# Performance work log

Measured on AMD Instinct MI355X. Metric: run time of the kernel, lower is better.

The kernel has to match this reference:

```python
import jax, jax.numpy as jnp
import numpy as np

N_NODES = 100000
N_EDGES = 3200000
IN_DIM, HID_DIM, OUT_DIM = 64, 16, 2


def setup_inputs() -> dict:
    key = jax.random.key(0)
    ks = jax.random.split(key, 6)
    x = jax.random.normal(ks[0], (N_NODES, IN_DIM), dtype=jnp.float32)
    edge_index = jax.random.randint(ks[1], (2, N_EDGES), 0, N_NODES, dtype=jnp.int64)
    W1 = jax.random.normal(ks[2], (IN_DIM, HID_DIM), dtype=jnp.float32) * (1.0 / np.sqrt(IN_DIM))
    b1 = jax.random.normal(ks[3], (HID_DIM,), dtype=jnp.float32) * 0.01
    W2 = jax.random.normal(ks[4], (HID_DIM, OUT_DIM), dtype=jnp.float32) * (1.0 / np.sqrt(HID_DIM))
    b2 = jax.random.normal(ks[5], (OUT_DIM,), dtype=jnp.float32) * 0.01
    return {"x": x, "edge_index": edge_index, "W1": W1, "b1": b1, "W2": W2, "b2": b2}


def _gcn_conv(x, src, dst, W, b, n_nodes):
    """PyG GCNConv: add self-loops, symmetric norm, linear, scatter-add, bias."""
    h = x @ W  # [N, out]
    loop = jnp.arange(n_nodes, dtype=src.dtype)
    s = jnp.concatenate([src, loop])  # [E+N]
    d = jnp.concatenate([dst, loop])
    deg = jax.ops.segment_sum(jnp.ones_like(d, dtype=h.dtype), d, num_segments=n_nodes)
    dinv = jnp.where(deg > 0, jax.lax.rsqrt(deg), 0.0)
    norm = dinv[s] * dinv[d]  # [E+N]
    msgs = h[s] * norm[:, None]  # gather + scale
    out = jax.ops.segment_sum(msgs, d, num_segments=n_nodes)
    return out + b


def reference(x, edge_index, W1, b1, W2, b2):
    src, dst = edge_index[0], edge_index[1]
    h = _gcn_conv(x, src, dst, W1, b1, N_NODES)
    h = jax.nn.relu(h)
    h = _gcn_conv(h, src, dst, W2, b2, N_NODES)
    return jax.nn.log_softmax(h, axis=1)
```

## Files before the change

### kernel.cpp

```cpp
#include <hip/hip_runtime.h>
#include <math.h>
#include <stdint.h>

#define N_NODES 100000
#define N_EDGES 3200000
#define IN_DIM  64
#define HID     16
#define OUTD    2

#define NPAD    100352
#define B_CHUNKS 128
#define CHUNK_E  (N_EDGES / B_CHUNKS)
#define NB       256
#define BK_NODES (NPAD / NB)
#define BK_CAP   14336

#define OFF_DINV  0
#define OFF_RS    (OFF_DINV + NPAD)
#define OFF_RE    (OFF_RS + NPAD)
#define OFF_H1    (OFF_RE + NPAD)
#define OFF_H2    (OFF_H1 + N_NODES * HID)
#define OFF_CSR   (OFF_H2 + N_NODES * OUTD)
#define OFF_PAIRS (OFF_CSR + N_EDGES)
#define OFF_HCNT  (OFF_PAIRS + 2 * N_EDGES)
#define OFF_BST   (OFF_HCNT + B_CHUNKS * NB)


__global__ __launch_bounds__(256) void k_bhist(const int* __restrict__ dst,
                                               unsigned* __restrict__ hcnt) {
    __shared__ unsigned h[NB];
    h[threadIdx.x] = 0u;
    __syncthreads();
    int base = blockIdx.x * CHUNK_E;
    for (int i = threadIdx.x; i < CHUNK_E; i += 256)
        atomicAdd(&h[dst[base + i] / BK_NODES], 1u);
    __syncthreads();
    hcnt[blockIdx.x * NB + threadIdx.x] = h[threadIdx.x];
}

__global__ __launch_bounds__(256) void k_bscan(unsigned* __restrict__ hcnt,
                                               int* __restrict__ bstart) {
    int bk = threadIdx.x, lane = bk & 63, wid = bk >> 6;
    int tot = 0;
    for (int b = 0; b < B_CHUNKS; b++) tot += (int)hcnt[(size_t)b * NB + bk];
    int x = tot;
#pragma unroll
    for (int off = 1; off < 64; off <<= 1) {
        int y = __shfl_up(x, off, 64);
        if (lane >= off) x += y;
    }
    __shared__ int wt[4];
    if (lane == 63) wt[wid] = x;
    __syncthreads();
    int wb = 0;
#pragma unroll
    for (int w = 0; w < 4; w++) if (w < wid) wb += wt[w];
    int start = wb + x - tot;
    bstart[bk] = start;
    if (bk == NB - 1) bstart[NB] = start + tot;
    unsigned run = (unsigned)start;
    for (int b = 0; b < B_CHUNKS; b++) {
        unsigned c = hcnt[(size_t)b * NB + bk];
        hcnt[(size_t)b * NB + bk] = run;
        run += c;
    }
}

__global__ __launch_bounds__(256) void k_bscatter(
    const int* __restrict__ src, const int* __restrict__ dst,
    const unsigned* __restrict__ hcnt, unsigned long long* __restrict__ pairs) {
    __shared__ unsigned cur[NB];
    cur[threadIdx.x] = hcnt[(size_t)blockIdx.x * NB + threadIdx.x];
    __syncthreads();
    int base = blockIdx.x * CHUNK_E;
    for (int i = threadIdx.x; i < CHUNK_E; i += 256) {
        int e = base + i;
        int d = dst[e];
        unsigned pos = atomicAdd(&cur[d / BK_NODES], 1u);
        pairs[pos] = ((unsigned long long)(unsigned)src[e] << 32) | (unsigned)d;
    }
}

__global__ __launch_bounds__(256) void k_bsort(
    const unsigned long long* __restrict__ pairs, const int* __restrict__ bstart,
    int* __restrict__ csr, int* __restrict__ rs, int* __restrict__ re,
    float* __restrict__ dinv) {
    __shared__ unsigned long long lp[BK_CAP];
    __shared__ unsigned cnt[BK_NODES];
    __shared__ unsigned rstart[BK_NODES];
    int bk = blockIdx.x;
    int s0 = bstart[bk], s1 = bstart[bk + 1];
    int ne = s1 - s0;
    if (ne > BK_CAP) ne = BK_CAP;
    for (int i = threadIdx.x; i < ne; i += 256) lp[i] = pairs[s0 + i];
    for (int i = threadIdx.x; i < BK_NODES; i += 256) cnt[i] = 0u;
    __syncthreads();
    int nlo = bk * BK_NODES;
    for (int i = threadIdx.x; i < ne; i += 256) {
        int dl = (int)(unsigned)(lp[i] & 0xffffffffu) - nlo;
        atomicAdd(&cnt[dl], 1u);
    }
    __syncthreads();
    if (threadIdx.x < 64) {
        int lane = threadIdx.x;
        unsigned loc[7];
        unsigned s = 0;
#pragma unroll
        for (int q = 0; q < 7; q++) {
            int idx = lane * 7 + q;
            unsigned c = (idx < BK_NODES) ? cnt[idx] : 0u;
            loc[q] = s; s += c;
        }
        unsigned x = s;
#pragma unroll
        for (int off = 1; off < 64; off <<= 1) {
            unsigned y = __shfl_up((int)x, off, 64);
            if (lane >= off) x += y;
        }
        unsigned basev = x - s;
#pragma unroll
        for (int q = 0; q < 7; q++) {
            int idx = lane * 7 + q;
            if (idx < BK_NODES) rstart[idx] = basev + loc[q];
        }
    }
    __syncthreads();
    for (int i = threadIdx.x; i < BK_NODES; i += 256) {
        int n = nlo + i;
        unsigned st = rstart[i], en = st + cnt[i];
        rs[n] = s0 + (int)st;
        re[n] = s0 + (int)en;
        dinv[n] = rsqrtf((float)(cnt[i] + 1));
    }
    __syncthreads();
    for (int i = threadIdx.x; i < ne; i += 256) {
        unsigned long long p = lp[i];
        int dl = (int)(unsigned)(p & 0xffffffffu) - nlo;
        unsigned pos = atomicAdd(&rstart[dl], 1u);
        csr[s0 + (int)pos] = (int)(unsigned)(p >> 32);
    }
}


__global__ void k_lin1s(const float* __restrict__ x, const float* __restrict__ W1,
                        const float* __restrict__ dinv, float* __restrict__ h1s) {
    __shared__ float w[IN_DIM * HID];
    for (int i = threadIdx.x; i < IN_DIM * HID; i += blockDim.x) w[i] = W1[i];
    __syncthreads();
    int n = blockIdx.x * blockDim.x + threadIdx.x;
    if (n >= N_NODES) return;
    float acc[HID];
#pragma unroll
    for (int j = 0; j < HID; j++) acc[j] = 0.f;
    const float4* xr = (const float4*)(x + (size_t)n * IN_DIM);
#pragma unroll
    for (int k4 = 0; k4 < IN_DIM / 4; k4++) {
        float4 v = xr[k4];
#pragma unroll
        for (int j = 0; j < HID; j++) {
            acc[j] += v.x * w[(k4 * 4 + 0) * HID + j]
                    + v.y * w[(k4 * 4 + 1) * HID + j]
                    + v.z * w[(k4 * 4 + 2) * HID + j]
                    + v.w * w[(k4 * 4 + 3) * HID + j];
        }
    }
    float di = dinv[n];
    float4* o = (float4*)(h1s + (size_t)n * HID);
    o[0] = make_float4(di * acc[0], di * acc[1], di * acc[2], di * acc[3]);
    o[1] = make_float4(di * acc[4], di * acc[5], di * acc[6], di * acc[7]);
    o[2] = make_float4(di * acc[8], di * acc[9], di * acc[10], di * acc[11]);
    o[3] = make_float4(di * acc[12], di * acc[13], di * acc[14], di * acc[15]);
}

__global__ __launch_bounds__(256) void k_pull1(
    const int* __restrict__ rs, const int* __restrict__ re,
    const int* __restrict__ csr, const float* __restrict__ h1s,
    const float* __restrict__ dinv, const float* __restrict__ b1,
    const float* __restrict__ W2, float* __restrict__ h2s) {
    int n = blockIdx.x * 4 + (threadIdx.x >> 6);
    if (n >= N_NODES) return;
    int lane = threadIdx.x & 63;
    int es = lane >> 4, j = lane & 15;
    int beg = rs[n], end = re[n];
    float acc = 0.f;
    for (int i = beg + es; i < end; i += 4) {
        int s = csr[i];
        acc += h1s[(size_t)s * HID + j];
    }
    acc += __shfl_xor(acc, 16, 64);
    acc += __shfl_xor(acc, 32, 64);
    float di = dinv[n];
    float v = fmaxf(di * (acc + h1s[(size_t)n * HID + j]) + b1[j], 0.f);
    float p0 = v * W2[j * 2 + 0];
    float p1 = v * W2[j * 2 + 1];
#pragma unroll
    for (int m = 1; m <= 8; m <<= 1) {
        p0 += __shfl_xor(p0, m, 64);
        p1 += __shfl_xor(p1, m, 64);
    }
    if (lane == 0) *(float2*)(h2s + (size_t)n * 2) = make_float2(di * p0, di * p1);
}

__global__ __launch_bounds__(256) void k_pull2(
    const int* __restrict__ rs, const int* __restrict__ re,
    const int* __restrict__ csr, const float* __restrict__ h2s,
    const float* __restrict__ dinv, const float* __restrict__ b2,
    float* __restrict__ out) {
    int n = blockIdx.x * 4 + (threadIdx.x >> 6);
    if (n >= N_NODES) return;
    int lane = threadIdx.x & 63;
    int e = lane >> 1, k = lane & 1;
    int beg = rs[n], end = re[n];
    float acc = 0.f;
    for (int i = beg + e; i < end; i += 32) {
        int s = csr[i];
        acc += h2s[(size_t)s * 2 + k];
    }
#pragma unroll
    for (int m = 2; m <= 32; m <<= 1) acc += __shfl_xor(acc, m, 64);
    float di = dinv[n];
    float o = di * (acc + h2s[(size_t)n * 2 + k]) + b2[k];
    float other = __shfl_xor(o, 1, 64);
    float mx = fmaxf(o, other);
    float lse = mx + logf(expf(o - mx) + expf(other - mx));
    if (lane < 2) out[(size_t)n * 2 + k] = o - lse;
}

extern "C" void kernel_launch(void* const* d_in, const int* in_sizes, int n_in,
                              void* d_out, int out_size, void* d_ws, size_t ws_size,
                              hipStream_t stream) {
    const float* x  = (const float*)d_in[0];
    const int*   ei = (const int*)d_in[1];
    const int*   srcv = ei;
    const int*   dstv = ei + N_EDGES;
    const float* W1 = (const float*)d_in[2];
    const float* b1 = (const float*)d_in[3];
    const float* W2 = (const float*)d_in[4];
    const float* b2 = (const float*)d_in[5];
    float* out = (float*)d_out;

    float*              ws     = (float*)d_ws;
    float*              dinv   = ws + OFF_DINV;
    int*                rs     = (int*)(ws + OFF_RS);
    int*                re     = (int*)(ws + OFF_RE);
    float*              h1s    = ws + OFF_H1;
    float*              h2s    = ws + OFF_H2;
    int*                csr    = (int*)(ws + OFF_CSR);
    unsigned long long* pairs  = (unsigned long long*)(ws + OFF_PAIRS);
    unsigned*           hcnt   = (unsigned*)(ws + OFF_HCNT);
    int*                bstart = (int*)(ws + OFF_BST);

    k_bhist<<<B_CHUNKS, 256, 0, stream>>>(dstv, hcnt);
    k_bscan<<<1, 256, 0, stream>>>(hcnt, bstart);
    k_bscatter<<<B_CHUNKS, 256, 0, stream>>>(srcv, dstv, hcnt, pairs);
    k_bsort<<<NB, 256, 0, stream>>>(pairs, bstart, csr, rs, re, dinv);
    k_lin1s<<<(N_NODES + 255) / 256, 256, 0, stream>>>(x, W1, dinv, h1s);
    k_pull1<<<(N_NODES + 3) / 4, 256, 0, stream>>>(rs, re, csr, h1s, dinv, b1, W2, h2s);
    k_pull2<<<(N_NODES + 3) / 4, 256, 0, stream>>>(rs, re, csr, h2s, dinv, b2, out);
}
```

Baseline: 329.0 us.

## Pack bucket pairs into 32 bits, double buckets, store layer-1 features as bf16

Raises the bucket count from 256 to 512 so each bucket holds 196 nodes. Each (src, local dst) pair now packs into one 32-bit word with an 8-bit local index, which halves scatter and sort traffic and shared-memory use. The layer-1 hidden features are stored as packed bf16 with round-to-nearest-even. This halves the bytes fetched per gathered neighbour in the first aggregation, where each lane now accumulates two features. The bf16 storage reduces precision of the aggregated features, and the 8-bit src shift limits source ids to 24 bits, which is enough here.

Measured after the change: 396.5 us. 20.5% more time.

```diff
diff --git a/kernel.cpp b/kernel.cpp
--- a/kernel.cpp
+++ b/kernel.cpp
@@ -8,37 +8,45 @@
 #define HID     16
 #define OUTD    2
 
-#define NPAD    100352
+#define NPAD     100352
 #define B_CHUNKS 128
 #define CHUNK_E  (N_EDGES / B_CHUNKS)
-#define NB       256
+#define NB       512
 #define BK_NODES (NPAD / NB)
-#define BK_CAP   14336
+#define BK_CAP   7680
 
 #define OFF_DINV  0
 #define OFF_RS    (OFF_DINV + NPAD)
 #define OFF_RE    (OFF_RS + NPAD)
-#define OFF_H1    (OFF_RE + NPAD)
-#define OFF_H2    (OFF_H1 + N_NODES * HID)
+#define OFF_H1B   (OFF_RE + NPAD)
+#define OFF_H2    (OFF_H1B + N_NODES * 8)
 #define OFF_CSR   (OFF_H2 + N_NODES * OUTD)
 #define OFF_PAIRS (OFF_CSR + N_EDGES)
-#define OFF_HCNT  (OFF_PAIRS + 2 * N_EDGES)
+#define OFF_HCNT  (OFF_PAIRS + N_EDGES)
 #define OFF_BST   (OFF_HCNT + B_CHUNKS * NB)
+
+__device__ __forceinline__ unsigned packbf2(float f0, float f1) {
+    unsigned a = __float_as_uint(f0), b = __float_as_uint(f1);
+    a = (a + 0x7fffu + ((a >> 16) & 1u)) >> 16;
+    b = (b + 0x7fffu + ((b >> 16) & 1u)) >> 16;
+    return a | (b << 16);
+}
 
 
 __global__ __launch_bounds__(256) void k_bhist(const int* __restrict__ dst,
                                                unsigned* __restrict__ hcnt) {
     __shared__ unsigned h[NB];
-    h[threadIdx.x] = 0u;
+    for (int i = threadIdx.x; i < NB; i += 256) h[i] = 0u;
     __syncthreads();
     int base = blockIdx.x * CHUNK_E;
     for (int i = threadIdx.x; i < CHUNK_E; i += 256)
         atomicAdd(&h[dst[base + i] / BK_NODES], 1u);
     __syncthreads();
-    hcnt[blockIdx.x * NB + threadIdx.x] = h[threadIdx.x];
-}
-
-__global__ __launch_bounds__(256) void k_bscan(unsigned* __restrict__ hcnt,
+    for (int i = threadIdx.x; i < NB; i += 256)
+        hcnt[(size_t)blockIdx.x * NB + i] = h[i];
+}
+
+__global__ __launch_bounds__(512) void k_bscan(unsigned* __restrict__ hcnt,
                                                int* __restrict__ bstart) {
     int bk = threadIdx.x, lane = bk & 63, wid = bk >> 6;
     int tot = 0;
@@ -49,12 +57,12 @@
         int y = __shfl_up(x, off, 64);
         if (lane >= off) x += y;
     }
-    __shared__ int wt[4];
+    __shared__ int wt[8];
     if (lane == 63) wt[wid] = x;
     __syncthreads();
     int wb = 0;
 #pragma unroll
-    for (int w = 0; w < 4; w++) if (w < wid) wb += wt[w];
+    for (int w = 0; w < 8; w++) if (w < wid) wb += wt[w];
     int start = wb + x - tot;
     bstart[bk] = start;
     if (bk == NB - 1) bstart[NB] = start + tot;
@@ -68,24 +76,26 @@
 
 __global__ __launch_bounds__(256) void k_bscatter(
     const int* __restrict__ src, const int* __restrict__ dst,
-    const unsigned* __restrict__ hcnt, unsigned long long* __restrict__ pairs) {
+    const unsigned* __restrict__ hcnt, unsigned* __restrict__ pairs) {
     __shared__ unsigned cur[NB];
-    cur[threadIdx.x] = hcnt[(size_t)blockIdx.x * NB + threadIdx.x];
+    for (int i = threadIdx.x; i < NB; i += 256)
+        cur[i] = hcnt[(size_t)blockIdx.x * NB + i];
     __syncthreads();
     int base = blockIdx.x * CHUNK_E;
     for (int i = threadIdx.x; i < CHUNK_E; i += 256) {
         int e = base + i;
         int d = dst[e];
-        unsigned pos = atomicAdd(&cur[d / BK_NODES], 1u);
-        pairs[pos] = ((unsigned long long)(unsigned)src[e] << 32) | (unsigned)d;
+        int bk = d / BK_NODES;
+        unsigned pos = atomicAdd(&cur[bk], 1u);
+        pairs[pos] = ((unsigned)src[e] << 8) | (unsigned)(d - bk * BK_NODES);
     }
 }
 
 __global__ __launch_bounds__(256) void k_bsort(
-    const unsigned long long* __restrict__ pairs, const int* __restrict__ bstart,
+    const unsigned* __restrict__ pairs, const int* __restrict__ bstart,
     int* __restrict__ csr, int* __restrict__ rs, int* __restrict__ re,
     float* __restrict__ dinv) {
-    __shared__ unsigned long long lp[BK_CAP];
+    __shared__ unsigned lp[BK_CAP];
     __shared__ unsigned cnt[BK_NODES];
     __shared__ unsigned rstart[BK_NODES];
     int bk = blockIdx.x;
@@ -95,19 +105,16 @@
     for (int i = threadIdx.x; i < ne; i += 256) lp[i] = pairs[s0 + i];
     for (int i = threadIdx.x; i < BK_NODES; i += 256) cnt[i] = 0u;
     __syncthreads();
-    int nlo = bk * BK_NODES;
-    for (int i = threadIdx.x; i < ne; i += 256) {
-        int dl = (int)(unsigned)(lp[i] & 0xffffffffu) - nlo;
-        atomicAdd(&cnt[dl], 1u);
-    }
+    for (int i = threadIdx.x; i < ne; i += 256)
+        atomicAdd(&cnt[lp[i] & 0xffu], 1u);
     __syncthreads();
     if (threadIdx.x < 64) {
         int lane = threadIdx.x;
-        unsigned loc[7];
+        unsigned loc[4];
         unsigned s = 0;
 #pragma unroll
-        for (int q = 0; q < 7; q++) {
-            int idx = lane * 7 + q;
+        for (int q = 0; q < 4; q++) {
+            int idx = lane * 4 + q;
             unsigned c = (idx < BK_NODES) ? cnt[idx] : 0u;
             loc[q] = s; s += c;
         }
@@ -119,31 +126,31 @@
         }
         unsigned basev = x - s;
 #pragma unroll
-        for (int q = 0; q < 7; q++) {
-            int idx = lane * 7 + q;
+        for (int q = 0; q < 4; q++) {
+            int idx = lane * 4 + q;
             if (idx < BK_NODES) rstart[idx] = basev + loc[q];
         }
     }
     __syncthreads();
+    int nlo = bk * BK_NODES;
     for (int i = threadIdx.x; i < BK_NODES; i += 256) {
         int n = nlo + i;
-        unsigned st = rstart[i], en = st + cnt[i];
+        unsigned st = rstart[i];
         rs[n] = s0 + (int)st;
-        re[n] = s0 + (int)en;
+        re[n] = s0 + (int)(st + cnt[i]);
         dinv[n] = rsqrtf((float)(cnt[i] + 1));
     }
     __syncthreads();
     for (int i = threadIdx.x; i < ne; i += 256) {
-        unsigned long long p = lp[i];
-        int dl = (int)(unsigned)(p & 0xffffffffu) - nlo;
-        unsigned pos = atomicAdd(&rstart[dl], 1u);
-        csr[s0 + (int)pos] = (int)(unsigned)(p >> 32);
+        unsigned p = lp[i];
+        unsigned pos = atomicAdd(&rstart[p & 0xffu], 1u);
+        csr[s0 + (int)pos] = (int)(p >> 8);
     }
 }
 
 
 __global__ void k_lin1s(const float* __restrict__ x, const float* __restrict__ W1,
-                        const float* __restrict__ dinv, float* __restrict__ h1s) {
+                        const float* __restrict__ dinv, unsigned* __restrict__ h1b) {
     __shared__ float w[IN_DIM * HID];
     for (int i = threadIdx.x; i < IN_DIM * HID; i += blockDim.x) w[i] = W1[i];
     __syncthreads();
@@ -165,39 +172,52 @@
         }
     }
     float di = dinv[n];
-    float4* o = (float4*)(h1s + (size_t)n * HID);
-    o[0] = make_float4(di * acc[0], di * acc[1], di * acc[2], di * acc[3]);
-    o[1] = make_float4(di * acc[4], di * acc[5], di * acc[6], di * acc[7]);
-    o[2] = make_float4(di * acc[8], di * acc[9], di * acc[10], di * acc[11]);
-    o[3] = make_float4(di * acc[12], di * acc[13], di * acc[14], di * acc[15]);
+    uint4 o0, o1;
+    o0.x = packbf2(di * acc[0],  di * acc[1]);
+    o0.y = packbf2(di * acc[2],  di * acc[3]);
+    o0.z = packbf2(di * acc[4],  di * acc[5]);
+    o0.w = packbf2(di * acc[6],  di * acc[7]);
+    o1.x = packbf2(di * acc[8],  di * acc[9]);
+    o1.y = packbf2(di * acc[10], di * acc[11]);
+    o1.z = packbf2(di * acc[12], di * acc[13]);
+    o1.w = packbf2(di * acc[14], di * acc[15]);
+    uint4* o = (uint4*)(h1b + (size_t)n * 8);
+    o[0] = o0;
+    o[1] = o1;
 }
 
 __global__ __launch_bounds__(256) void k_pull1(
     const int* __restrict__ rs, const int* __restrict__ re,
-    const int* __restrict__ csr, const float* __restrict__ h1s,
+    const int* __restrict__ csr, const unsigned* __restrict__ h1b,
     const float* __restrict__ dinv, const float* __restrict__ b1,
     const float* __restrict__ W2, float* __restrict__ h2s) {
     int n = blockIdx.x * 4 + (threadIdx.x >> 6);
     if (n >= N_NODES) return;
     int lane = threadIdx.x & 63;
-    int es = lane >> 4, j = lane & 15;
+    int slot = lane >> 3, w = lane & 7;
     int beg = rs[n], end = re[n];
-    float acc = 0.f;
-    for (int i = beg + es; i < end; i += 4) {
+    float a0 = 0.f, a1 = 0.f;
+    for (int i = beg + slot; i < end; i += 8) {
         int s = csr[i];
-        acc += h1s[(size_t)s * HID + j];
-    }
-    acc += __shfl_xor(acc, 16, 64);
-    acc += __shfl_xor(acc, 32, 64);
+        unsigned u = h1b[(size_t)s * 8 + w];
+        a0 += __uint_as_float(u << 16);
+        a1 += __uint_as_float(u & 0xffff0000u);
+    }
+    a0 += __shfl_xor(a0, 8, 64);  a1 += __shfl_xor(a1, 8, 64);
+    a0 += __shfl_xor(a0, 16, 64); a1 += __shfl_xor(a1, 16, 64);
+    a0 += __shfl_xor(a0, 32, 64); a1 += __shfl_xor(a1, 32, 64);
+    unsigned us = h1b[(size_t)n * 8 + w];
+    a0 += __uint_as_float(us << 16);
+    a1 += __uint_as_float(us & 0xffff0000u);
     float di = dinv[n];
-    float v = fmaxf(di * (acc + h1s[(size_t)n * HID + j]) + b1[j], 0.f);
-    float p0 = v * W2[j * 2 + 0];
-    float p1 = v * W2[j * 2 + 1];
-#pragma unroll
-    for (int m = 1; m <= 8; m <<= 1) {
-        p0 += __shfl_xor(p0, m, 64);
-        p1 += __shfl_xor(p1, m, 64);
-    }
+    int j0 = 2 * w, j1 = 2 * w + 1;
+    float v0 = fmaxf(di * a0 + b1[j0], 0.f);
+    float v1 = fmaxf(di * a1 + b1[j1], 0.f);
+    float p0 = v0 * W2[j0 * 2 + 0] + v1 * W2[j1 * 2 + 0];
+    float p1 = v0 * W2[j0 * 2 + 1] + v1 * W2[j1 * 2 + 1];
+    p0 += __shfl_xor(p0, 1, 64); p1 += __shfl_xor(p1, 1, 64);
+    p0 += __shfl_xor(p0, 2, 64); p1 += __shfl_xor(p1, 2, 64);
+    p0 += __shfl_xor(p0, 4, 64); p1 += __shfl_xor(p1, 4, 64);
     if (lane == 0) *(float2*)(h2s + (size_t)n * 2) = make_float2(di * p0, di * p1);
 }
 
@@ -239,22 +259,22 @@
     const float* b2 = (const float*)d_in[5];
     float* out = (float*)d_out;
 
-    float*              ws     = (float*)d_ws;
-    float*              dinv   = ws + OFF_DINV;
-    int*                rs     = (int*)(ws + OFF_RS);
-    int*                re     = (int*)(ws + OFF_RE);
-    float*              h1s    = ws + OFF_H1;
-    float*              h2s    = ws + OFF_H2;
-    int*                csr    = (int*)(ws + OFF_CSR);
-    unsigned long long* pairs  = (unsigned long long*)(ws + OFF_PAIRS);
-    unsigned*           hcnt   = (unsigned*)(ws + OFF_HCNT);
-    int*                bstart = (int*)(ws + OFF_BST);
+    float*    ws     = (float*)d_ws;
+    float*    dinv   = ws + OFF_DINV;
+    int*      rs     = (int*)(ws + OFF_RS);
+    int*      re     = (int*)(ws + OFF_RE);
+    unsigned* h1b    = (unsigned*)(ws + OFF_H1B);
+    float*    h2s    = ws + OFF_H2;
+    int*      csr    = (int*)(ws + OFF_CSR);
+    unsigned* pairs  = (unsigned*)(ws + OFF_PAIRS);
+    unsigned* hcnt   = (unsigned*)(ws + OFF_HCNT);
+    int*      bstart = (int*)(ws + OFF_BST);
 
     k_bhist<<<B_CHUNKS, 256, 0, stream>>>(dstv, hcnt);
-    k_bscan<<<1, 256, 0, stream>>>(hcnt, bstart);
+    k_bscan<<<1, 512, 0, stream>>>(hcnt, bstart);
     k_bscatter<<<B_CHUNKS, 256, 0, stream>>>(srcv, dstv, hcnt, pairs);
     k_bsort<<<NB, 256, 0, stream>>>(pairs, bstart, csr, rs, re, dinv);
-    k_lin1s<<<(N_NODES + 255) / 256, 256, 0, stream>>>(x, W1, dinv, h1s);
-    k_pull1<<<(N_NODES + 3) / 4, 256, 0, stream>>>(rs, re, csr, h1s, dinv, b1, W2, h2s);
+    k_lin1s<<<(N_NODES + 255) / 256, 256, 0, stream>>>(x, W1, dinv, h1b);
+    k_pull1<<<(N_NODES + 3) / 4, 256, 0, stream>>>(rs, re, csr, h1b, dinv, b1, W2, h2s);
     k_pull2<<<(N_NODES + 3) / 4, 256, 0, stream>>>(rs, re, csr, h2s, dinv, b2, out);
 }
```
